# Kernel optimization log

Hardware: AMD Instinct MI355X
Metric: run time of the kernel (lower is better)

Reference implementation:

```python
import jax, jax.numpy as jnp
import numpy as np

SIZE = 512

def _corner_means(x):
    # x: [B, C, H, W]; top-left corner nested-shell means via integral image.
    cs = jnp.cumsum(jnp.cumsum(x, axis=2), axis=3)          # [B, C, H, W]
    d = jnp.diagonal(cs, axis1=2, axis2=3)[..., :SIZE]      # [B, C, SIZE] = sum of i x i corner window
    shell = jnp.concatenate([d[..., :1], d[..., 1:] - d[..., :-1]], axis=-1)
    counts = (2 * jnp.arange(1, SIZE + 1) - 1).astype(x.dtype)  # i*i - (i-1)*(i-1)
    return shell / counts                                    # [B, C, SIZE]

def setup_inputs() -> dict:
    key = jax.random.key(0)
    x = jax.random.normal(key, (32, 8, 512, 512), dtype=jnp.float32)
    return {"x": x}

def reference(x):
    tl = _corner_means(x)
    tr = _corner_means(x[:, :, :, ::-1])
    bl = _corner_means(x[:, :, ::-1, :])
    br = _corner_means(x[:, :, ::-1, ::-1])
    # each [B, C, SIZE] -> [B, SIZE, C]; concat corners on channel dim -> [B, SIZE, 4C]
    out = jnp.concatenate(
        [jnp.swapaxes(t, 1, 2) for t in (tl, tr, bl, br)], axis=2
    )
    return out
```

## Files before the change

kernel.cpp:

```cpp
#include <hip/hip_runtime.h>


#define PLANES 256
#define WW     512
#define HH     512
#define JBLK   8
#define RPB    64

__device__ __forceinline__ float wave_sum64(float v) {
  v += __int_as_float(__builtin_amdgcn_update_dpp(0, __float_as_int(v), 0x111, 0xf, 0xf, true));
  v += __int_as_float(__builtin_amdgcn_update_dpp(0, __float_as_int(v), 0x112, 0xf, 0xf, true));
  v += __int_as_float(__builtin_amdgcn_update_dpp(0, __float_as_int(v), 0x114, 0xf, 0xf, true));
  v += __int_as_float(__builtin_amdgcn_update_dpp(0, __float_as_int(v), 0x118, 0xf, 0xf, true));
  v += __int_as_float(__builtin_amdgcn_update_dpp(0, __float_as_int(v), 0x142, 0xf, 0xf, true));
  v += __int_as_float(__builtin_amdgcn_update_dpp(0, __float_as_int(v), 0x143, 0xf, 0xf, true));
  return v;
}

__global__ __launch_bounds__(128, 4)
void corner_pass1(const float* __restrict__ x, float* __restrict__ wsA,
                  float* __restrict__ wsBT) {
  const int t     = threadIdx.x;
  const int plane = blockIdx.y;
  const int jb    = blockIdx.x;
  const int r0    = jb * RPB;

  const float4* base = (const float4*)(x + (size_t)plane * HH * WW + (size_t)r0 * WW);

  __shared__ float4 part[2][2];
  __shared__ float  slotA[2], slotB[2];

  float cs0 = 0.f, cs1 = 0.f, cs2 = 0.f, cs3 = 0.f;

  float4 v  = base[t];
  float4 v1 = base[128 + t];
  const int wv  = t >> 6;
  const int l63 = ((t & 63) == 63);
  const int c0  = t << 2;

  for (int rr = 0; rr < RPB; ++rr) {
    const int r = r0 + rr;
    const int q = 511 - r;

    float4 v2;
    if (rr + 2 < RPB) v2 = base[(rr + 2) * 128 + t];
    else              v2 = make_float4(0.f, 0.f, 0.f, 0.f);

    cs0 += v.x; cs1 += v.y; cs2 += v.z; cs3 += v.w;

    const float p0 = v.x, p1 = p0 + v.y, p2 = p1 + v.z, p3 = p2 + v.w;

    const int lt1 = (r - 1) - c0;
    const int lt2 = q - c0;
    float m1 = lt1 < 0 ? 0.f : (lt1 == 0 ? p0 : (lt1 == 1 ? p1 : (lt1 == 2 ? p2 : p3)));
    float m2 = lt2 < 0 ? 0.f : (lt2 == 0 ? p0 : (lt2 == 1 ? p1 : (lt2 == 2 ? p2 : p3)));
    float T  = p3;

    T  = wave_sum64(T);
    m1 = wave_sum64(m1);
    m2 = wave_sum64(m2);

    const int par = rr & 1;
    if (l63) part[par][wv] = make_float4(T, m1, m2, 0.f);

    if (t == (r >> 2)) {
      const int k = r & 3;
      slotA[par] = (k == 0 ? cs0 : k == 1 ? cs1 : k == 2 ? cs2 : cs3);
    }
    if (t == (q >> 2)) {
      const int k = q & 3;
      slotB[par] = (k == 0 ? cs0 : k == 1 ? cs1 : k == 2 ? cs2 : cs3);
    }

    __syncthreads();

    if (t == 0) {
      const float4 pa = part[par][0], pb = part[par][1];
      const float Ts = pa.x + pb.x;
      const float M1 = pa.y + pb.y;
      const float M2 = pa.z + pb.z;
      const float a  = slotA[par];
      const float b  = slotB[par];
      float4 A;
      A.x = M1 + a;
      A.y = Ts - M2 + b;
      A.z = M2 - b;
      A.w = Ts - M1 - a;
      ((float4*)wsA)[(size_t)plane * 512 + r] = A;
    }

    v = v1; v1 = v2;
  }

  float4* bt = (float4*)(wsBT + ((size_t)plane * JBLK + jb) * WW);
  bt[t] = make_float4(cs0, cs1, cs2, cs3);
}

__global__ __launch_bounds__(256)
void corner_pass2(const float* __restrict__ wsA, const float* __restrict__ wsBT,
                  float* __restrict__ out) {
  const int idx   = blockIdx.x * 256 + threadIdx.x;
  const int plane = idx >> 9;
  const int r     = idx & 511;
  const int q     = 511 - r;

  const float4 A  = ((const float4*)wsA)[idx];
  const float* bt = wsBT + (size_t)plane * JBLK * 512;

  const int jb = r >> 6;
  float prev_r = 0.f, tot_r = 0.f, prev_q = 0.f, tot_q = 0.f;
#pragma unroll
  for (int jj = 0; jj < JBLK; ++jj) {
    const float br_ = bt[jj * 512 + r];
    const float bq_ = bt[jj * 512 + q];
    tot_r += br_; tot_q += bq_;
    if (jj < jb) { prev_r += br_; prev_q += bq_; }
  }

  const float TL = A.x + prev_r;
  const float TR = A.y + prev_q;
  const float BL = A.z + (tot_q - prev_q);
  const float BR = A.w + (tot_r - prev_r);

  const float invr = 1.0f / (float)(2 * r + 1);
  const float invq = 1.0f / (float)(2 * q + 1);

  const int b = plane >> 3, c = plane & 7;
  float* ob = out + (size_t)b * 512 * 32;
  ob[r * 32 + c]      = TL * invr;
  ob[r * 32 + 8 + c]  = TR * invr;
  ob[q * 32 + 16 + c] = BL * invq;
  ob[q * 32 + 24 + c] = BR * invq;
}

extern "C" void kernel_launch(void* const* d_in, const int* in_sizes, int n_in,
                              void* d_out, int out_size, void* d_ws, size_t ws_size,
                              hipStream_t stream) {
  const float* x = (const float*)d_in[0];
  float* out = (float*)d_out;

  float* wsA  = (float*)d_ws;
  float* wsBT = wsA + (size_t)PLANES * 512 * 4;

  dim3 g1(JBLK, PLANES);
  corner_pass1<<<g1, 128, 0, stream>>>(x, wsA, wsBT);
  corner_pass2<<<512, 256, 0, stream>>>(wsA, wsBT, out);
}
```

Baseline: 368.2 us.

## Give each wavefront its own row strip and drop block-level syncs

Pass 1 now has each 64-lane wavefront own a 32-row strip across the full 512-wide row. Each lane handles 8 columns, so the row reduction completes within one wave using DPP sums and a shuffle. The per-row shared-memory handoff and __syncthreads are gone, and a 4-deep register prefetch ring replaces the 2-deep one. Row blocks double to 16, so pass 2 reads twice as many block totals, and register pressure rises from the 8-wide column state and the prefetch buffers.

```diff
diff --git a/kernel.cpp b/kernel.cpp
--- a/kernel.cpp
+++ b/kernel.cpp
@@ -4,8 +4,10 @@
 #define PLANES 256
 #define WW     512
 #define HH     512
-#define JBLK   8
-#define RPB    64
+#define JBLK   16
+#define RPB    32
+#define WPB    4
+#define PF     4
 
 __device__ __forceinline__ float wave_sum64(float v) {
   v += __int_as_float(__builtin_amdgcn_update_dpp(0, __float_as_int(v), 0x111, 0xf, 0xf, true));
@@ -17,83 +19,93 @@
   return v;
 }
 
-__global__ __launch_bounds__(128, 4)
+__global__ __launch_bounds__(256, 4)
 void corner_pass1(const float* __restrict__ x, float* __restrict__ wsA,
                   float* __restrict__ wsBT) {
   const int t     = threadIdx.x;
+  const int lane  = t & 63;
+  const int wv    = t >> 6;
   const int plane = blockIdx.y;
-  const int jb    = blockIdx.x;
+  const int jb    = blockIdx.x * WPB + wv;
   const int r0    = jb * RPB;
+  const int c0    = lane << 3;
 
   const float4* base = (const float4*)(x + (size_t)plane * HH * WW + (size_t)r0 * WW);
+  const int li = lane * 2;
 
-  __shared__ float4 part[2][2];
-  __shared__ float  slotA[2], slotB[2];
+  float4 b0[PF], b1[PF];
+#pragma unroll
+  for (int i = 0; i < PF; ++i) {
+    b0[i] = base[i * 128 + li];
+    b1[i] = base[i * 128 + li + 1];
+  }
 
-  float cs0 = 0.f, cs1 = 0.f, cs2 = 0.f, cs3 = 0.f;
+  float cs[8] = {0.f, 0.f, 0.f, 0.f, 0.f, 0.f, 0.f, 0.f};
 
-  float4 v  = base[t];
-  float4 v1 = base[128 + t];
-  const int wv  = t >> 6;
-  const int l63 = ((t & 63) == 63);
-  const int c0  = t << 2;
-
+#pragma unroll 4
   for (int rr = 0; rr < RPB; ++rr) {
     const int r = r0 + rr;
     const int q = 511 - r;
 
-    float4 v2;
-    if (rr + 2 < RPB) v2 = base[(rr + 2) * 128 + t];
-    else              v2 = make_float4(0.f, 0.f, 0.f, 0.f);
+    const float4 va = b0[rr & (PF - 1)];
+    const float4 vb = b1[rr & (PF - 1)];
+    if (rr + PF < RPB) {
+      b0[rr & (PF - 1)] = base[(rr + PF) * 128 + li];
+      b1[rr & (PF - 1)] = base[(rr + PF) * 128 + li + 1];
+    }
 
-    cs0 += v.x; cs1 += v.y; cs2 += v.z; cs3 += v.w;
+    cs[0] += va.x; cs[1] += va.y; cs[2] += va.z; cs[3] += va.w;
+    cs[4] += vb.x; cs[5] += vb.y; cs[6] += vb.z; cs[7] += vb.w;
 
-    const float p0 = v.x, p1 = p0 + v.y, p2 = p1 + v.z, p3 = p2 + v.w;
+    const float p0 = va.x, p1 = p0 + va.y, p2 = p1 + va.z, p3 = p2 + va.w;
+    const float p4 = p3 + vb.x, p5 = p4 + vb.y, p6 = p5 + vb.z, p7 = p6 + vb.w;
 
     const int lt1 = (r - 1) - c0;
     const int lt2 = q - c0;
-    float m1 = lt1 < 0 ? 0.f : (lt1 == 0 ? p0 : (lt1 == 1 ? p1 : (lt1 == 2 ? p2 : p3)));
-    float m2 = lt2 < 0 ? 0.f : (lt2 == 0 ? p0 : (lt2 == 1 ? p1 : (lt2 == 2 ? p2 : p3)));
-    float T  = p3;
+    float m1 = 0.f;
+    m1 = (lt1 >= 0) ? p0 : m1; m1 = (lt1 >= 1) ? p1 : m1;
+    m1 = (lt1 >= 2) ? p2 : m1; m1 = (lt1 >= 3) ? p3 : m1;
+    m1 = (lt1 >= 4) ? p4 : m1; m1 = (lt1 >= 5) ? p5 : m1;
+    m1 = (lt1 >= 6) ? p6 : m1; m1 = (lt1 >= 7) ? p7 : m1;
+    float m2 = 0.f;
+    m2 = (lt2 >= 0) ? p0 : m2; m2 = (lt2 >= 1) ? p1 : m2;
+    m2 = (lt2 >= 2) ? p2 : m2; m2 = (lt2 >= 3) ? p3 : m2;
+    m2 = (lt2 >= 4) ? p4 : m2; m2 = (lt2 >= 5) ? p5 : m2;
+    m2 = (lt2 >= 6) ? p6 : m2; m2 = (lt2 >= 7) ? p7 : m2;
 
+    float T = p7;
     T  = wave_sum64(T);
     m1 = wave_sum64(m1);
     m2 = wave_sum64(m2);
 
-    const int par = rr & 1;
-    if (l63) part[par][wv] = make_float4(T, m1, m2, 0.f);
+    const int k1 = r & 7, k2 = q & 7;
+    float selA = cs[0];
+    selA = (k1 == 1) ? cs[1] : selA; selA = (k1 == 2) ? cs[2] : selA;
+    selA = (k1 == 3) ? cs[3] : selA; selA = (k1 == 4) ? cs[4] : selA;
+    selA = (k1 == 5) ? cs[5] : selA; selA = (k1 == 6) ? cs[6] : selA;
+    selA = (k1 == 7) ? cs[7] : selA;
+    float selB = cs[0];
+    selB = (k2 == 1) ? cs[1] : selB; selB = (k2 == 2) ? cs[2] : selB;
+    selB = (k2 == 3) ? cs[3] : selB; selB = (k2 == 4) ? cs[4] : selB;
+    selB = (k2 == 5) ? cs[5] : selB; selB = (k2 == 7) ? cs[7] : selB;
+    selB = (k2 == 6) ? cs[6] : selB;
 
-    if (t == (r >> 2)) {
-      const int k = r & 3;
-      slotA[par] = (k == 0 ? cs0 : k == 1 ? cs1 : k == 2 ? cs2 : cs3);
-    }
-    if (t == (q >> 2)) {
-      const int k = q & 3;
-      slotB[par] = (k == 0 ? cs0 : k == 1 ? cs1 : k == 2 ? cs2 : cs3);
-    }
+    const float a = __shfl(selA, r >> 3, 64);
+    const float b = __shfl(selB, q >> 3, 64);
 
-    __syncthreads();
-
-    if (t == 0) {
-      const float4 pa = part[par][0], pb = part[par][1];
-      const float Ts = pa.x + pb.x;
-      const float M1 = pa.y + pb.y;
-      const float M2 = pa.z + pb.z;
-      const float a  = slotA[par];
-      const float b  = slotB[par];
+    if (lane == 63) {
       float4 A;
-      A.x = M1 + a;
-      A.y = Ts - M2 + b;
-      A.z = M2 - b;
-      A.w = Ts - M1 - a;
+      A.x = m1 + a;
+      A.y = T - m2 + b;
+      A.z = m2 - b;
+      A.w = T - m1 - a;
       ((float4*)wsA)[(size_t)plane * 512 + r] = A;
     }
-
-    v = v1; v1 = v2;
   }
 
-  float4* bt = (float4*)(wsBT + ((size_t)plane * JBLK + jb) * WW);
-  bt[t] = make_float4(cs0, cs1, cs2, cs3);
+  float4* bt = (float4*)(wsBT + ((size_t)plane * JBLK + jb) * WW + c0);
+  bt[0] = make_float4(cs[0], cs[1], cs[2], cs[3]);
+  bt[1] = make_float4(cs[4], cs[5], cs[6], cs[7]);
 }
 
 __global__ __launch_bounds__(256)
@@ -107,7 +119,7 @@
   const float4 A  = ((const float4*)wsA)[idx];
   const float* bt = wsBT + (size_t)plane * JBLK * 512;
 
-  const int jb = r >> 6;
+  const int jb = r >> 5;
   float prev_r = 0.f, tot_r = 0.f, prev_q = 0.f, tot_q = 0.f;
 #pragma unroll
   for (int jj = 0; jj < JBLK; ++jj) {
@@ -142,7 +154,7 @@
   float* wsA  = (float*)d_ws;
   float* wsBT = wsA + (size_t)PLANES * 512 * 4;
 
-  dim3 g1(JBLK, PLANES);
-  corner_pass1<<<g1, 128, 0, stream>>>(x, wsA, wsBT);
+  dim3 g1(JBLK / WPB, PLANES);
+  corner_pass1<<<g1, 256, 0, stream>>>(x, wsA, wsBT);
   corner_pass2<<<512, 256, 0, stream>>>(wsA, wsBT, out);
 }
```

Result: no change. 366.6 us (-0.4%).
